# Performance work log

Measured on AMD Instinct MI355X. Metric: run time of the kernel, lower is better.

The kernel has to match this reference:

```python
import jax, jax.numpy as jnp
import numpy as np


def _log_adjacency(feats, temperature):
    """'ours' euclidean adjacency: -pairwise_dist * exp(temperature), row log_softmax."""
    B = feats.shape[0]
    f = feats.reshape(B, -1)                      # (B, D)
    diff = f[:, None, :] - f[None, :, :]          # (B, B, D) as in the torch code
    sq = jnp.sum(diff * diff, axis=-1)            # (B, B) squared distances
    # safe sqrt: zero distance on the diagonal, zero (sub)gradient like torch norm
    dist = jnp.where(sq > 0, jnp.sqrt(jnp.where(sq > 0, sq, 1.0)), 0.0)
    pre_softmax = -dist * jnp.exp(temperature)
    return jax.nn.log_softmax(pre_softmax, axis=1)


def setup_inputs() -> dict:
    key = jax.random.key(0)
    k1, k2 = jax.random.split(key)
    B, C, P, D = 128, 64, 32, 128
    image_feats = jax.random.normal(k1, (B, C, D), dtype=jnp.float32)
    lang_feats = jax.random.normal(k2, (B, P, D), dtype=jnp.float32)
    temperature = jnp.float32(np.log(0.5))  # learnable temperature param init
    return {"image_feats": image_feats, "lang_feats": lang_feats, "temperature": temperature}


def reference(image_feats, lang_feats, temperature):
    A_f = _log_adjacency(image_feats, temperature)   # (B, B) log-probs
    A_g = _log_adjacency(lang_feats, temperature)    # (B, B) log-probs (log target)
    # F.kl_div(A_f, A_g, log_target=True, reduction='none') = exp(A_g) * (A_g - A_f)
    kl = jnp.exp(A_g) * (A_g - A_f)
    return kl.sum(axis=0)                            # (B,)
```

## Files before the change

kernel.cpp:

```cpp
#include <hip/hip_runtime.h>
#include <hip/hip_bf16.h>
#include <math.h>


#define NROW 128
#define PAIRS 16384
#define D0 8192
#define D1 4096
#define NC0 128
#define NC1 64
#define NCHUNK 192
#define ROWSTRIDE 140

__device__ __forceinline__ int swz(int r) { return r + ((r >> 5) << 2); }

__global__ __launch_bounds__(256) void k_gram(
    const float* __restrict__ F0, const float* __restrict__ F1,
    float* __restrict__ partials, float* __restrict__ diagP,
    float* __restrict__ out)
{
    __shared__ float lds[64 * ROWSTRIDE];

    const int b = blockIdx.x;
    const int t = threadIdx.x;
    if (b == 0 && t < NROW) out[t] = 0.0f;

    const float* F; int D, chunk;
    if (b < NC0) { F = F0; D = D0; chunk = b; }
    else         { F = F1; D = D1; chunk = b - NC0; }
    const int k0 = chunk * 64;

    {
        const int rr = t >> 4;
        const int c4 = (t & 15) * 4;
#pragma unroll
        for (int it = 0; it < 8; ++it) {
            const int r = it * 16 + rr;
            const float4 v = *(const float4*)(F + (size_t)r * D + k0 + c4);
            const int p = swz(r);
            lds[(c4 + 0) * ROWSTRIDE + p] = v.x;
            lds[(c4 + 1) * ROWSTRIDE + p] = v.y;
            lds[(c4 + 2) * ROWSTRIDE + p] = v.z;
            lds[(c4 + 3) * ROWSTRIDE + p] = v.w;
        }
    }
    __syncthreads();

    const int ti = t >> 4, tj = t & 15;
    const int i0 = ti * 8, j0 = tj * 8;
    const int ia = swz(i0);
    const int ib = swz(j0);

    float acc[8][8];
#pragma unroll
    for (int p = 0; p < 8; ++p)
#pragma unroll
        for (int q = 0; q < 8; ++q) acc[p][q] = 0.0f;

#pragma unroll 8
    for (int k = 0; k < 64; ++k) {
        const float* row = lds + k * ROWSTRIDE;
        const float4 a0 = *(const float4*)(row + ia);
        const float4 a1 = *(const float4*)(row + ia + 4);
        const float4 b0 = *(const float4*)(row + ib);
        const float4 b1 = *(const float4*)(row + ib + 4);
        const float a[8]  = {a0.x, a0.y, a0.z, a0.w, a1.x, a1.y, a1.z, a1.w};
        const float bb[8] = {b0.x, b0.y, b0.z, b0.w, b1.x, b1.y, b1.z, b1.w};
#pragma unroll
        for (int p = 0; p < 8; ++p)
#pragma unroll
            for (int q = 0; q < 8; ++q)
                acc[p][q] = fmaf(a[p], bb[q], acc[p][q]);
    }

    float* __restrict__ pout = partials + (size_t)b * PAIRS;
#pragma unroll
    for (int p = 0; p < 8; ++p) {
        float4* dst = (float4*)(pout + (i0 + p) * NROW + j0);
        dst[0] = make_float4(acc[p][0], acc[p][1], acc[p][2], acc[p][3]);
        dst[1] = make_float4(acc[p][4], acc[p][5], acc[p][6], acc[p][7]);
    }
    if (ti == tj) {
        float* dd = diagP + b * NROW + i0;
#pragma unroll
        for (int p = 0; p < 8; ++p) dd[p] = acc[p][p];
    }
}

__device__ __forceinline__ float waveMax64(float v) {
#pragma unroll
    for (int off = 32; off > 0; off >>= 1) v = fmaxf(v, __shfl_xor(v, off, 64));
    return v;
}
__device__ __forceinline__ float waveSum64(float v) {
#pragma unroll
    for (int off = 32; off > 0; off >>= 1) v += __shfl_xor(v, off, 64);
    return v;
}
__device__ __forceinline__ float blockMax128(float v, float* red) {
    v = waveMax64(v);
    if ((threadIdx.x & 63) == 0) red[threadIdx.x >> 6] = v;
    __syncthreads();
    const float r = fmaxf(red[0], red[1]);
    __syncthreads();
    return r;
}
__device__ __forceinline__ float blockSum128(float v, float* red) {
    v = waveSum64(v);
    if ((threadIdx.x & 63) == 0) red[threadIdx.x >> 6] = v;
    __syncthreads();
    const float r = red[0] + red[1];
    __syncthreads();
    return r;
}

__global__ __launch_bounds__(128) void k_kl(
    const float* __restrict__ partials, const float* __restrict__ diagP,
    const float* __restrict__ temp, float* __restrict__ out)
{
    __shared__ float diag[NROW];
    __shared__ float red[2];
    const int i = blockIdx.x;
    const int j = threadIdx.x;
    const float et = expf(temp[0]);

    float A[2];
#pragma unroll
    for (int s = 0; s < 2; ++s) {
        const float* Ps = partials + (s ? (size_t)NC0 * PAIRS : 0);
        const float* Ds = diagP + (s ? NC0 * NROW : 0);
        const int nc = s ? NC1 : NC0;

        float gij = 0.0f, gjj = 0.0f;
        for (int c = 0; c < nc; ++c) {
            gij += Ps[c * PAIRS + i * NROW + j];
            gjj += Ds[c * NROW + j];
        }
        diag[j] = gjj;
        __syncthreads();
        const float gii = diag[i];
        __syncthreads();

        const float sq = gii + gjj - 2.0f * gij;
        const float dist = sq > 0.0f ? sqrtf(sq) : 0.0f;
        const float pre = -dist * et;
        const float m = blockMax128(pre, red);
        const float ssum = blockSum128(expf(pre - m), red);
        A[s] = pre - (m + logf(ssum));
    }
    const float kl = expf(A[1]) * (A[1] - A[0]);
    atomicAdd(out + j, kl);
}

extern "C" void kernel_launch(void* const* d_in, const int* in_sizes, int n_in,
                              void* d_out, int out_size, void* d_ws, size_t ws_size,
                              hipStream_t stream)
{
    const float* img  = (const float*)d_in[0];
    const float* lng  = (const float*)d_in[1];
    const float* temp = (const float*)d_in[2];
    float* out = (float*)d_out;

    float* partials = (float*)d_ws;
    float* diagP    = partials + (size_t)NCHUNK * PAIRS;

    k_gram<<<NCHUNK, 256, 0, stream>>>(img, lng, partials, diagP, out);
    k_kl<<<NROW, NROW, 0, stream>>>(partials, diagP, temp, out);
}
```

Baseline: 85.16 us.

## Use bf16x3 split MFMA for Gram chunks and parallelize KL reduction over both adjacencies

The Gram kernel drops the LDS-transposed FP32 FMA outer product. Each wave now loads fragments straight from global memory, splits each float into bf16 hi and lo parts, and accumulates with four 32x32x16 bf16 MFMAs per tile to approximate FP32 accuracy. The KL kernel uses 256 threads so the image and language adjacencies are reduced at the same time, with 4-way unrolled partial sums and an exact zero on the diagonal. This gains matrix-core throughput and more parallelism in the reduction. The cost is bf16-split rounding error, uncoalesced direct global loads, and scalar partial stores.

```diff
diff --git a/kernel.cpp b/kernel.cpp
--- a/kernel.cpp
+++ b/kernel.cpp
@@ -7,84 +7,108 @@
 #define PAIRS 16384
 #define D0 8192
 #define D1 4096
+#define CK 64
 #define NC0 128
 #define NC1 64
 #define NCHUNK 192
-#define ROWSTRIDE 140
-
-__device__ __forceinline__ int swz(int r) { return r + ((r >> 5) << 2); }
+
+typedef short v8s  __attribute__((ext_vector_type(8)));
+typedef float v16f __attribute__((ext_vector_type(16)));
+
+union Frag {
+    v8s s;
+    __hip_bfloat162 h[4];
+};
+
+__device__ __forceinline__ void splitPair(float a, float b, Frag& hi, Frag& lo, int idx) {
+    __hip_bfloat162 h = __float22bfloat162_rn(make_float2(a, b));
+    const float ra = a - __bfloat162float(h.x);
+    const float rb = b - __bfloat162float(h.y);
+    __hip_bfloat162 l = __float22bfloat162_rn(make_float2(ra, rb));
+    hi.h[idx] = h;
+    lo.h[idx] = l;
+}
+
+__device__ __forceinline__ void loadFrag(const float* __restrict__ p, Frag& hi, Frag& lo) {
+    const float4 v0 = *(const float4*)(p);
+    const float4 v1 = *(const float4*)(p + 4);
+    splitPair(v0.x, v0.y, hi, lo, 0);
+    splitPair(v0.z, v0.w, hi, lo, 1);
+    splitPair(v1.x, v1.y, hi, lo, 2);
+    splitPair(v1.z, v1.w, hi, lo, 3);
+}
 
 __global__ __launch_bounds__(256) void k_gram(
     const float* __restrict__ F0, const float* __restrict__ F1,
     float* __restrict__ partials, float* __restrict__ diagP,
     float* __restrict__ out)
 {
-    __shared__ float lds[64 * ROWSTRIDE];
-
     const int b = blockIdx.x;
     const int t = threadIdx.x;
     if (b == 0 && t < NROW) out[t] = 0.0f;
 
-    const float* F; int D, chunk;
-    if (b < NC0) { F = F0; D = D0; chunk = b; }
-    else         { F = F1; D = D1; chunk = b - NC0; }
-    const int k0 = chunk * 64;
-
-    {
-        const int rr = t >> 4;
-        const int c4 = (t & 15) * 4;
-#pragma unroll
-        for (int it = 0; it < 8; ++it) {
-            const int r = it * 16 + rr;
-            const float4 v = *(const float4*)(F + (size_t)r * D + k0 + c4);
-            const int p = swz(r);
-            lds[(c4 + 0) * ROWSTRIDE + p] = v.x;
-            lds[(c4 + 1) * ROWSTRIDE + p] = v.y;
-            lds[(c4 + 2) * ROWSTRIDE + p] = v.z;
-            lds[(c4 + 3) * ROWSTRIDE + p] = v.w;
+    const float* F; int D, k0;
+    if (b < NC0) { F = F0; D = D0; k0 = b * CK; }
+    else         { F = F1; D = D1; k0 = (b - NC0) * CK; }
+
+    const int wave  = t >> 6;
+    const int wy    = wave >> 1;
+    const int wx    = wave & 1;
+    const int lane  = t & 63;
+    const int r32   = lane & 31;
+    const int khalf = lane >> 5;
+
+    const int rA0 = wy * 64 + r32;
+    const int rA1 = wy * 64 + 32 + r32;
+    const int rB0 = wx * 64 + r32;
+    const int rB1 = wx * 64 + 32 + r32;
+
+    v16f acc[2][2];
+#pragma unroll
+    for (int ti = 0; ti < 2; ++ti)
+#pragma unroll
+        for (int tj = 0; tj < 2; ++tj)
+#pragma unroll
+            for (int r = 0; r < 16; ++r) acc[ti][tj][r] = 0.0f;
+
+#pragma unroll
+    for (int g = 0; g < CK / 16; ++g) {
+        const int col = k0 + g * 16 + khalf * 8;
+        Frag Ah[2], Al[2], Bh[2], Bl[2];
+        loadFrag(F + (size_t)rA0 * D + col, Ah[0], Al[0]);
+        loadFrag(F + (size_t)rA1 * D + col, Ah[1], Al[1]);
+        loadFrag(F + (size_t)rB0 * D + col, Bh[0], Bl[0]);
+        loadFrag(F + (size_t)rB1 * D + col, Bh[1], Bl[1]);
+#pragma unroll
+        for (int ti = 0; ti < 2; ++ti)
+#pragma unroll
+            for (int tj = 0; tj < 2; ++tj) {
+                acc[ti][tj] = __builtin_amdgcn_mfma_f32_32x32x16_bf16(
+                    Ah[ti].s, Bh[tj].s, acc[ti][tj], 0, 0, 0);
+                acc[ti][tj] = __builtin_amdgcn_mfma_f32_32x32x16_bf16(
+                    Ah[ti].s, Bl[tj].s, acc[ti][tj], 0, 0, 0);
+                acc[ti][tj] = __builtin_amdgcn_mfma_f32_32x32x16_bf16(
+                    Al[ti].s, Bh[tj].s, acc[ti][tj], 0, 0, 0);
+                acc[ti][tj] = __builtin_amdgcn_mfma_f32_32x32x16_bf16(
+                    Al[ti].s, Bl[tj].s, acc[ti][tj], 0, 0, 0);
+            }
+    }
+
+    float* __restrict__ pout = partials + (size_t)b * PAIRS;
+#pragma unroll
+    for (int ti = 0; ti < 2; ++ti)
+#pragma unroll
+        for (int tj = 0; tj < 2; ++tj) {
+            const int rowbase = wy * 64 + ti * 32;
+            const int n = wx * 64 + tj * 32 + r32;
+#pragma unroll
+            for (int r = 0; r < 16; ++r) {
+                const int m = rowbase + (r & 3) + 8 * (r >> 2) + 4 * khalf;
+                const float v = acc[ti][tj][r];
+                pout[m * NROW + n] = v;
+                if (m == n) diagP[b * NROW + m] = v;
+            }
         }
-    }
-    __syncthreads();
-
-    const int ti = t >> 4, tj = t & 15;
-    const int i0 = ti * 8, j0 = tj * 8;
-    const int ia = swz(i0);
-    const int ib = swz(j0);
-
-    float acc[8][8];
-#pragma unroll
-    for (int p = 0; p < 8; ++p)
-#pragma unroll
-        for (int q = 0; q < 8; ++q) acc[p][q] = 0.0f;
-
-#pragma unroll 8
-    for (int k = 0; k < 64; ++k) {
-        const float* row = lds + k * ROWSTRIDE;
-        const float4 a0 = *(const float4*)(row + ia);
-        const float4 a1 = *(const float4*)(row + ia + 4);
-        const float4 b0 = *(const float4*)(row + ib);
-        const float4 b1 = *(const float4*)(row + ib + 4);
-        const float a[8]  = {a0.x, a0.y, a0.z, a0.w, a1.x, a1.y, a1.z, a1.w};
-        const float bb[8] = {b0.x, b0.y, b0.z, b0.w, b1.x, b1.y, b1.z, b1.w};
-#pragma unroll
-        for (int p = 0; p < 8; ++p)
-#pragma unroll
-            for (int q = 0; q < 8; ++q)
-                acc[p][q] = fmaf(a[p], bb[q], acc[p][q]);
-    }
-
-    float* __restrict__ pout = partials + (size_t)b * PAIRS;
-#pragma unroll
-    for (int p = 0; p < 8; ++p) {
-        float4* dst = (float4*)(pout + (i0 + p) * NROW + j0);
-        dst[0] = make_float4(acc[p][0], acc[p][1], acc[p][2], acc[p][3]);
-        dst[1] = make_float4(acc[p][4], acc[p][5], acc[p][6], acc[p][7]);
-    }
-    if (ti == tj) {
-        float* dd = diagP + b * NROW + i0;
-#pragma unroll
-        for (int p = 0; p < 8; ++p) dd[p] = acc[p][p];
-    }
 }
 
 __device__ __forceinline__ float waveMax64(float v) {
@@ -97,59 +121,80 @@
     for (int off = 32; off > 0; off >>= 1) v += __shfl_xor(v, off, 64);
     return v;
 }
-__device__ __forceinline__ float blockMax128(float v, float* red) {
-    v = waveMax64(v);
-    if ((threadIdx.x & 63) == 0) red[threadIdx.x >> 6] = v;
-    __syncthreads();
-    const float r = fmaxf(red[0], red[1]);
-    __syncthreads();
-    return r;
-}
-__device__ __forceinline__ float blockSum128(float v, float* red) {
-    v = waveSum64(v);
-    if ((threadIdx.x & 63) == 0) red[threadIdx.x >> 6] = v;
-    __syncthreads();
-    const float r = red[0] + red[1];
-    __syncthreads();
-    return r;
-}
-
-__global__ __launch_bounds__(128) void k_kl(
+
+__global__ __launch_bounds__(256) void k_kl(
     const float* __restrict__ partials, const float* __restrict__ diagP,
     const float* __restrict__ temp, float* __restrict__ out)
 {
-    __shared__ float diag[NROW];
-    __shared__ float red[2];
+    __shared__ float red[4];
+    __shared__ float gii_s[2];
+    __shared__ float Arow[2][NROW];
+
     const int i = blockIdx.x;
-    const int j = threadIdx.x;
+    const int t = threadIdx.x;
+    const int s = t >> 7;
+    const int j = t & 127;
+    const int w = t >> 6;
     const float et = expf(temp[0]);
 
-    float A[2];
-#pragma unroll
-    for (int s = 0; s < 2; ++s) {
-        const float* Ps = partials + (s ? (size_t)NC0 * PAIRS : 0);
-        const float* Ds = diagP + (s ? NC0 * NROW : 0);
-        const int nc = s ? NC1 : NC0;
-
-        float gij = 0.0f, gjj = 0.0f;
-        for (int c = 0; c < nc; ++c) {
-            gij += Ps[c * PAIRS + i * NROW + j];
-            gjj += Ds[c * NROW + j];
+    const int   base = s ? NC0 : 0;
+    const int   nc   = s ? NC1 : NC0;
+    const float* Ps  = partials + (size_t)base * PAIRS;
+    const float* Ds  = diagP + base * NROW;
+
+    float a0 = 0.f, a1 = 0.f, a2 = 0.f, a3 = 0.f;
+    {
+        const float* p = Ps + i * NROW + j;
+        for (int c = 0; c < nc; c += 4) {
+            a0 += p[(size_t)(c + 0) * PAIRS];
+            a1 += p[(size_t)(c + 1) * PAIRS];
+            a2 += p[(size_t)(c + 2) * PAIRS];
+            a3 += p[(size_t)(c + 3) * PAIRS];
         }
-        diag[j] = gjj;
-        __syncthreads();
-        const float gii = diag[i];
-        __syncthreads();
-
-        const float sq = gii + gjj - 2.0f * gij;
-        const float dist = sq > 0.0f ? sqrtf(sq) : 0.0f;
-        const float pre = -dist * et;
-        const float m = blockMax128(pre, red);
-        const float ssum = blockSum128(expf(pre - m), red);
-        A[s] = pre - (m + logf(ssum));
-    }
-    const float kl = expf(A[1]) * (A[1] - A[0]);
-    atomicAdd(out + j, kl);
+    }
+    const float gij = (a0 + a1) + (a2 + a3);
+
+    float d0 = 0.f, d1 = 0.f, d2 = 0.f, d3 = 0.f;
+    {
+        const float* p = Ds + j;
+        for (int c = 0; c < nc; c += 4) {
+            d0 += p[(c + 0) * NROW];
+            d1 += p[(c + 1) * NROW];
+            d2 += p[(c + 2) * NROW];
+            d3 += p[(c + 3) * NROW];
+        }
+    }
+    const float gjj = (d0 + d1) + (d2 + d3);
+
+    if (j == i) gii_s[s] = gjj;
+    __syncthreads();
+    const float gii = gii_s[s];
+
+    const float sq   = (i == j) ? 0.0f : (gii + gjj - 2.0f * gij);
+    const float dist = sq > 0.0f ? sqrtf(sq) : 0.0f;
+    const float pre  = -dist * et;
+
+    float m = waveMax64(pre);
+    if ((t & 63) == 0) red[w] = m;
+    __syncthreads();
+    m = fmaxf(red[2 * s], red[2 * s + 1]);
+    __syncthreads();
+
+    float e = expf(pre - m);
+    float sum = waveSum64(e);
+    if ((t & 63) == 0) red[w] = sum;
+    __syncthreads();
+    sum = red[2 * s] + red[2 * s + 1];
+
+    const float A = pre - (m + logf(sum));
+    Arow[s][j] = A;
+    __syncthreads();
+
+    if (s == 0) {
+        const float Af = Arow[0][j];
+        const float Ag = Arow[1][j];
+        atomicAdd(out + j, expf(Ag) * (Ag - Af));
+    }
 }
 
 extern "C" void kernel_launch(void* const* d_in, const int* in_sizes, int n_in,
@@ -165,5 +210,5 @@
     float* diagP    = partials + (size_t)NCHUNK * PAIRS;
 
     k_gram<<<NCHUNK, 256, 0, stream>>>(img, lng, partials, diagP, out);
-    k_kl<<<NROW, NROW, 0, stream>>>(partials, diagP, temp, out);
-}
+    k_kl<<<NROW, 256, 0, stream>>>(partials, diagP, temp, out);
+}
```

After: 87.90 us. +3.2%, slower.
